# Optimization experiments

Hardware: AMD Instinct MI355X
Metric: run time of the kernel (lower is better)

## Reference

```python
import jax, jax.numpy as jnp
import numpy as np

B, C, H, W = 2048, 512, 4, 4
T, D, NH, HD, FF, NL = 16, 512, 8, 64, 1024, 4
EPS = 1e-5
SCALE = float(1.0 / np.sqrt(HD))


def _make_adj(h, w):
    # torch_geometric.utils.grid(h, w): 3x3 neighborhood incl. self-loop;
    # GCNConv sym-normalizes: A_hat = D^-1/2 A D^-1/2
    n = h * w
    A = np.zeros((n, n), np.float32)
    for r in range(h):
        for c in range(w):
            for dr in (-1, 0, 1):
                for dc in (-1, 0, 1):
                    rr, cc = r + dr, c + dc
                    if 0 <= rr < h and 0 <= cc < w:
                        A[r * w + c, rr * w + cc] = 1.0
    dinv = 1.0 / np.sqrt(A.sum(1))
    return (A * dinv[:, None] * dinv[None, :]).astype(np.float32)


def setup_inputs():
    key = jax.random.key(0)
    ks = iter(jax.random.split(key, 64))
    def w(*s):
        return jax.random.normal(next(ks), s, jnp.float32) * 0.02
    return dict(
        x=jax.random.normal(next(ks), (B, C, H, W), jnp.float32),
        emb_w=w(D, D), emb_b=jnp.zeros((D,), jnp.float32),
        emb_ln_g=jnp.ones((D,), jnp.float32), emb_ln_b=jnp.zeros((D,), jnp.float32),
        pos=w(1, T, D),
        attn_wq=w(NL, D, D), attn_wk=w(NL, D, D), attn_wv=w(NL, D, D),
        attn_bq=jnp.zeros((NL, D), jnp.float32), attn_bk=jnp.zeros((NL, D), jnp.float32),
        attn_bv=jnp.zeros((NL, D), jnp.float32),
        attn_wo=w(NL, D, D), attn_bo=jnp.zeros((NL, D), jnp.float32),
        ln1_g=jnp.ones((NL, D), jnp.float32), ln1_b=jnp.zeros((NL, D), jnp.float32),
        ff_w1=w(NL, D, FF), ff_b1=jnp.zeros((NL, FF), jnp.float32),
        ff_w2=w(NL, FF, D), ff_b2=jnp.zeros((NL, D), jnp.float32),
        ln2_g=jnp.ones((NL, D), jnp.float32), ln2_b=jnp.zeros((NL, D), jnp.float32),
        fc_w=w(D, D), fc_b=jnp.zeros((D,), jnp.float32),
        fc_ln_g=jnp.ones((D,), jnp.float32), fc_ln_b=jnp.zeros((D,), jnp.float32),
        gcn_w1=w(C, 2 * C), gcn_b1=jnp.zeros((2 * C,), jnp.float32),
        gcn_ln1_g=jnp.ones((2 * C,), jnp.float32), gcn_ln1_b=jnp.zeros((2 * C,), jnp.float32),
        gcn_w2=w(2 * C, C), gcn_b2=jnp.zeros((C,), jnp.float32),
        gcn_ln2_g=jnp.ones((C,), jnp.float32), gcn_ln2_b=jnp.zeros((C,), jnp.float32),
        fusion_w=w(C, 2 * C), fusion_b=jnp.zeros((C,), jnp.float32),
        adj=jnp.asarray(_make_adj(H, W)),
    )


def _ln(x, g, b):
    mu = x.mean(-1, keepdims=True)
    var = ((x - mu) ** 2).mean(-1, keepdims=True)
    return (x - mu) * jax.lax.rsqrt(var + EPS) * g + b


def reference(x, emb_w, emb_b, emb_ln_g, emb_ln_b, pos,
              attn_wq, attn_wk, attn_wv, attn_bq, attn_bk, attn_bv, attn_wo, attn_bo,
              ln1_g, ln1_b, ff_w1, ff_b1, ff_w2, ff_b2, ln2_g, ln2_b,
              fc_w, fc_b, fc_ln_g, fc_ln_b,
              gcn_w1, gcn_b1, gcn_ln1_g, gcn_ln1_b, gcn_w2, gcn_b2, gcn_ln2_g, gcn_ln2_b,
              fusion_w, fusion_b, adj):
    Bx = x.shape[0]
    # ---- transformer branch: tokens = 16 spatial positions, dim 512 ----
    h = x.reshape(Bx, C, T).transpose(0, 2, 1)                 # [B,T,D]
    h = _ln(h @ emb_w + emb_b, emb_ln_g, emb_ln_b) + pos
    for i in range(NL):  # post-norm TransformerEncoderLayer, ReLU, eval (no dropout)
        q = (h @ attn_wq[i] + attn_bq[i]).reshape(Bx, T, NH, HD).transpose(0, 2, 1, 3)
        k = (h @ attn_wk[i] + attn_bk[i]).reshape(Bx, T, NH, HD).transpose(0, 2, 1, 3)
        v = (h @ attn_wv[i] + attn_bv[i]).reshape(Bx, T, NH, HD).transpose(0, 2, 1, 3)
        a = jax.nn.softmax(jnp.einsum('bhqd,bhkd->bhqk', q, k) * SCALE, axis=-1)
        o = jnp.einsum('bhqk,bhkd->bhqd', a, v).transpose(0, 2, 1, 3).reshape(Bx, T, D)
        h = _ln(h + o @ attn_wo[i] + attn_bo[i], ln1_g[i], ln1_b[i])
        f = jax.nn.relu(h @ ff_w1[i] + ff_b1[i]) @ ff_w2[i] + ff_b2[i]
        h = _ln(h + f, ln2_g[i], ln2_b[i])
    h = _ln(h @ fc_w + fc_b, fc_ln_g, fc_ln_b)
    x1 = h.transpose(0, 2, 1).reshape(Bx, C, H, W)
    # ---- GCN branch: dense normalized adjacency over the 16-node grid ----
    xn = x.transpose(0, 2, 3, 1).reshape(Bx, T, C)             # [B,16,C]
    g = jnp.einsum('mn,bnd->bmd', adj, xn @ gcn_w1) + gcn_b1   # GCNConv1 (bias after aggr)
    g = jax.nn.elu(_ln(g, gcn_ln1_g, gcn_ln1_b))
    g = jnp.einsum('mn,bnd->bmd', adj, g @ gcn_w2) + gcn_b2    # GCNConv2
    g = jax.nn.elu(_ln(g, gcn_ln2_g, gcn_ln2_b))
    x2 = g.reshape(Bx, H, W, C).transpose(0, 3, 1, 2)
    # ---- fusion: 1x1 conv + InstanceNorm2d (no affine) + ELU ----
    xc = jnp.concatenate([x1, x2], axis=1)                     # [B,2C,H,W]
    y = jnp.einsum('oc,bchw->bohw', fusion_w, xc) + fusion_b[None, :, None, None]
    mu = y.mean((2, 3), keepdims=True)
    var = ((y - mu) ** 2).mean((2, 3), keepdims=True)
    y = (y - mu) * jax.lax.rsqrt(var + EPS)
    return jax.nn.elu(y)
```

## Files before the change

kernel.cpp:

```cpp
#include <hip/hip_runtime.h>


typedef _Float16 f16;
typedef f16 f16x8 __attribute__((ext_vector_type(8)));
typedef f16 f16x4 __attribute__((ext_vector_type(4)));
typedef float f32x4 __attribute__((ext_vector_type(4)));

__device__ inline float wred_sum(float s) {
#pragma unroll
  for (int m = 32; m; m >>= 1) s += __shfl_xor(s, m);
  return s;
}

struct WDesc {
  const float* src;
  f16* dst;
  int K, N, tiles_n, tile_base, mode;
};
struct WTable {
  WDesc d[32];
  int n;
};

__global__ void wconvert_kernel(WTable tab) {
  const int tile = blockIdx.x;
  int di = 0;
  while (di + 1 < tab.n && tab.d[di + 1].tile_base <= tile) ++di;
  const WDesc w = tab.d[di];
  const int t = tile - w.tile_base;
  const int tk = t / w.tiles_n, tn = t % w.tiles_n;
  const int tid = threadIdx.x;
  const int rr = tid >> 5, cc = tid & 31;
  __shared__ float tb[32][33];
  if (w.mode == 0) {
#pragma unroll
    for (int i = 0; i < 4; i++) {
      const int k = tk * 32 + i * 8 + rr, n = tn * 32 + cc;
      tb[i * 8 + rr][cc] = w.src[(size_t)k * w.N + n];
    }
    __syncthreads();
#pragma unroll
    for (int i = 0; i < 4; i++) {
      const int n = tn * 32 + i * 8 + rr, k = tk * 32 + cc;
      w.dst[(size_t)n * w.K + k] = (f16)tb[cc][i * 8 + rr];
    }
  } else {
#pragma unroll
    for (int i = 0; i < 4; i++) {
      const int k = tk * 32 + i * 8 + rr, n = tn * 32 + cc;
      w.dst[(size_t)k * w.N + n] = (f16)w.src[(size_t)k * w.N + n];
    }
  }
}

__global__ void biaspack_kernel(const float* __restrict__ bq,
                                const float* __restrict__ bk,
                                const float* __restrict__ bv,
                                float* __restrict__ bqkv) {
  const int i = blockIdx.x * 256 + threadIdx.x;
  if (i >= 4 * 1536) return;
  const int l = i / 1536, j = i % 1536;
  float v;
  if (j < 512)       v = bq[l * 512 + j];
  else if (j < 1024) v = bk[l * 512 + j - 512];
  else               v = bv[l * 512 + j - 1024];
  bqkv[i] = v;
}

__global__ void prep_kernel(const float* __restrict__ x, f16* __restrict__ X0) {
  const int b = blockIdx.x;
  for (int c = threadIdx.x; c < 512; c += 256) {
    const float* src = x + ((size_t)b * 512 + c) * 16;
    float vals[16];
#pragma unroll
    for (int i = 0; i < 4; i++) {
      const float4 v = ((const float4*)src)[i];
      vals[i * 4 + 0] = v.x; vals[i * 4 + 1] = v.y;
      vals[i * 4 + 2] = v.z; vals[i * 4 + 3] = v.w;
    }
#pragma unroll
    for (int t = 0; t < 16; t++)
      X0[((size_t)b * 16 + t) * 512 + c] = (f16)vals[t];
  }
}

#define STAGE_SLOT(TI, ISB, HALF)                                              \
  {                                                                            \
    f16* dstb_ = smw + ((TI) & 1) * 32768 + ((ISB) ? 16384 : 0) +              \
                 (HALF) * 8192 + ldsw2;                                        \
    const int ld_ = (ISB) ? ldb : lda;                                         \
    const f16* src_ = ((ISB) ? gBs : gAs) + (size_t)((HALF) * 128) * ld_ +     \
                      ((size_t)(TI) << 6);                                     \
    __builtin_amdgcn_global_load_lds(                                          \
        (const __attribute__((address_space(1))) void*)(src_),                 \
        (__attribute__((address_space(3))) void*)(dstb_), 16, 0, 0);           \
    __builtin_amdgcn_global_load_lds(                                          \
        (const __attribute__((address_space(1))) void*)(src_ + (size_t)64 * ld_), \
        (__attribute__((address_space(3))) void*)(dstb_ + 4096), 16, 0, 0);    \
  }

#define VM4 asm volatile("s_waitcnt vmcnt(4)" ::: "memory");
#define VM0 asm volatile("s_waitcnt vmcnt(0)" ::: "memory");
#define VMN

#define PHASE(TI, P, FIRST, DOSTG, STI, SISB, SHALF, VM)                       \
  {                                                                            \
    const f16* Ab_ = smw + ((TI) & 1) * 32768;                                 \
    const f16* Bb_ = Ab_ + 16384;                                              \
    if (FIRST) {                                                               \
      _Pragma("unroll") for (int n = 0; n < 4; ++n) {                          \
        const int r = wn + n * 16 + rm;                                        \
        bf[n][0] = *(const f16x8*)(Bb_ + r * 64 + koff0);                      \
        bf[n][1] = *(const f16x8*)(Bb_ + r * 64 + koff1);                      \
      }                                                                        \
    }                                                                          \
    const int r0_ = wm + (2 * (P)) * 16 + rm;                                  \
    const f16x8 a0k0 = *(const f16x8*)(Ab_ + r0_ * 64 + koff0);                \
    const f16x8 a0k1 = *(const f16x8*)(Ab_ + r0_ * 64 + koff1);                \
    const f16x8 a1k0 = *(const f16x8*)(Ab_ + (r0_ + 16) * 64 + koff0);         \
    const f16x8 a1k1 = *(const f16x8*)(Ab_ + (r0_ + 16) * 64 + koff1);         \
    if (DOSTG) STAGE_SLOT(STI, SISB, SHALF)                                    \
    VM                                                                         \
    __builtin_amdgcn_s_barrier();                                              \
    asm volatile("s_waitcnt lgkmcnt(0)" ::: "memory");                         \
    __builtin_amdgcn_sched_barrier(0);                                         \
    __builtin_amdgcn_s_setprio(1);                                             \
    _Pragma("unroll") for (int n = 0; n < 4; ++n) {                            \
      acc[2 * (P)][n] = __builtin_amdgcn_mfma_f32_16x16x32_f16(                \
          a0k0, bf[n][0], acc[2 * (P)][n], 0, 0, 0);                           \
      acc[2 * (P)][n] = __builtin_amdgcn_mfma_f32_16x16x32_f16(                \
          a0k1, bf[n][1], acc[2 * (P)][n], 0, 0, 0);                           \
      acc[2 * (P) + 1][n] = __builtin_amdgcn_mfma_f32_16x16x32_f16(            \
          a1k0, bf[n][0], acc[2 * (P) + 1][n], 0, 0, 0);                       \
      acc[2 * (P) + 1][n] = __builtin_amdgcn_mfma_f32_16x16x32_f16(            \
          a1k1, bf[n][1], acc[2 * (P) + 1][n], 0, 0, 0);                       \
    }                                                                          \
    __builtin_amdgcn_s_setprio(0);                                             \
    __builtin_amdgcn_s_barrier();                                              \
    __builtin_amdgcn_sched_barrier(0);                                         \
  }

template <int OUT, bool RELU, bool HASB, int NT>
__global__ __launch_bounds__(512) void gemm256_kernel(
    const f16* __restrict__ A, const f16* __restrict__ Bt, void* __restrict__ C,
    const float* __restrict__ bias, const f16* __restrict__ resp,
    int N, int lda, int ldb) {
  __shared__ alignas(16) f16 smem[65536];
  f16* smw = smem;
  const int tid = threadIdx.x;
  const int nb = N >> 8;
  const int cpx = gridDim.x >> 3;
  const int wg = (blockIdx.x & 7) * cpx + (blockIdx.x >> 3);
  const int bx = wg % nb, by = wg / nb;
  const int row0 = by << 8, col0 = bx << 8;
  const int lane = tid & 63;
  const int wid = tid >> 6;
  const int wm = (wid >> 2) << 7;
  const int wn = (wid & 3) << 6;
  const int rm = lane & 15;
  const int kg = lane >> 4;
  const int key = rm & 7;
  const int koff0 = ((kg ^ key)) << 3;
  const int koff1 = (((4 + kg) ^ key)) << 3;
  const int schunk = (tid & 7) ^ ((tid >> 3) & 7);
  const f16* gAs = A + (size_t)(row0 + (tid >> 3)) * lda + (schunk << 3);
  const f16* gBs = Bt + (size_t)(col0 + (tid >> 3)) * ldb + (schunk << 3);
  const int ldsw2 = (tid & 0x1C0) << 3;
  f32x4 acc[8][4] = {};
  f16x8 bf[4][2];

  STAGE_SLOT(0, 0, 0)
  STAGE_SLOT(0, 0, 1)
  STAGE_SLOT(0, 1, 0)
  STAGE_SLOT(0, 1, 1)
  STAGE_SLOT(1, 1, 0)
  STAGE_SLOT(1, 1, 1)
  VM4
  __builtin_amdgcn_s_barrier();
  __builtin_amdgcn_sched_barrier(0);

#pragma unroll 1
  for (int j = 0; j < NT / 2 - 1; ++j) {
    const int u = 2 * j, v = u + 1, t2 = u + 2, t3 = u + 3;
    PHASE(u, 0, true,  true, v,  0, 0, VMN)
    PHASE(u, 1, false, true, v,  0, 1, VMN)
    PHASE(u, 2, false, true, t2, 1, 0, VMN)
    PHASE(u, 3, false, true, t2, 1, 1, VM4)
    PHASE(v, 0, true,  true, t2, 0, 0, VMN)
    PHASE(v, 1, false, true, t2, 0, 1, VMN)
    PHASE(v, 2, false, true, t3, 1, 0, VMN)
    PHASE(v, 3, false, true, t3, 1, 1, VM4)
  }
  {
    const int u = NT - 2, v = NT - 1;
    PHASE(u, 0, true,  true,  v, 0, 0, VMN)
    PHASE(u, 1, false, true,  v, 0, 1, VMN)
    PHASE(u, 2, false, false, 0, 0, 0, VMN)
    PHASE(u, 3, false, false, 0, 0, 0, VM0)
    PHASE(v, 0, true,  false, 0, 0, 0, VMN)
    PHASE(v, 1, false, false, 0, 0, 0, VMN)
    PHASE(v, 2, false, false, 0, 0, 0, VMN)
    PHASE(v, 3, false, false, 0, 0, 0, VMN)
  }

  const int cn = lane & 15;
  const int rg = (lane >> 4) << 2;
  if (OUT == 3) {
    float* out = (float*)C;
#pragma unroll
    for (int m = 0; m < 8; ++m) {
      const int bidx = (row0 >> 4) + (wm >> 4) + m;
#pragma unroll
      for (int n = 0; n < 4; ++n) {
        const int col = col0 + wn + n * 16 + cn;
        const float v0 = acc[m][n][0], v1 = acc[m][n][1];
        const float v2 = acc[m][n][2], v3 = acc[m][n][3];
        float s = v0 + v1 + v2 + v3;
        s += __shfl_xor(s, 16);
        s += __shfl_xor(s, 32);
        const float mu = s * (1.f / 16.f);
        float q = (v0 - mu) * (v0 - mu) + (v1 - mu) * (v1 - mu) +
                  (v2 - mu) * (v2 - mu) + (v3 - mu) * (v3 - mu);
        q += __shfl_xor(q, 16);
        q += __shfl_xor(q, 32);
        const float rstd = rsqrtf(q * (1.f / 16.f) + 1e-5f);
        float4 z;
        z.x = (v0 - mu) * rstd; z.x = z.x > 0.f ? z.x : expm1f(z.x);
        z.y = (v1 - mu) * rstd; z.y = z.y > 0.f ? z.y : expm1f(z.y);
        z.z = (v2 - mu) * rstd; z.z = z.z > 0.f ? z.z : expm1f(z.z);
        z.w = (v3 - mu) * rstd; z.w = z.w > 0.f ? z.w : expm1f(z.w);
        *(float4*)(out + ((size_t)bidx * 512 + col) * 16 + rg) = z;
      }
    }
  } else {
#pragma unroll
    for (int m = 0; m < 8; ++m) {
#pragma unroll
      for (int n = 0; n < 4; ++n) {
        const int col = col0 + wn + n * 16 + cn;
        const float bv = HASB ? bias[col] : 0.0f;
#pragma unroll
        for (int r = 0; r < 4; ++r) {
          const int row = row0 + wm + m * 16 + rg + r;
          float v = acc[m][n][r] + bv;
          if (OUT == 4) v += (float)resp[(size_t)row * N + col];
          if (RELU) v = v > 0.f ? v : 0.f;
          ((f16*)C)[(size_t)row * N + col] = (f16)v;
        }
      }
    }
  }
}

template <bool RES, bool POS>
__global__ void ln_kernel(const f16* in, const f16* res, const float* g,
                          const float* b, const float* pos, f16* out) {
  const int row = (blockIdx.x << 2) + (threadIdx.x >> 6);
  const int lane = threadIdx.x & 63;
  const int c0 = lane << 3;
  float v[8];
  const f16x8 xi = *(const f16x8*)(in + (size_t)row * 512 + c0);
  if (RES) {
    const f16x8 ri = *(const f16x8*)(res + (size_t)row * 512 + c0);
#pragma unroll
    for (int j = 0; j < 8; j++) v[j] = (float)xi[j] + (float)ri[j];
  } else {
#pragma unroll
    for (int j = 0; j < 8; j++) v[j] = (float)xi[j];
  }
  float s = 0;
#pragma unroll
  for (int j = 0; j < 8; j++) s += v[j];
  s = wred_sum(s);
  const float mu = s * (1.f / 512.f);
  float q = 0;
#pragma unroll
  for (int j = 0; j < 8; j++) {
    const float d = v[j] - mu;
    q += d * d;
  }
  q = wred_sum(q);
  const float rstd = rsqrtf(q * (1.f / 512.f) + 1e-5f);
  const int t = row & 15;
  f16x8 o8;
#pragma unroll
  for (int j = 0; j < 8; j++) {
    float o = (v[j] - mu) * rstd * g[c0 + j] + b[c0 + j];
    if (POS) o += pos[t * 512 + c0 + j];
    o8[j] = (f16)o;
  }
  *(f16x8*)(out + (size_t)row * 512 + c0) = o8;
}

__global__ void lnpack_kernel(const f16* __restrict__ in, const f16* __restrict__ x2,
                              const float* __restrict__ g, const float* __restrict__ b,
                              f16* __restrict__ F) {
  const int row = (blockIdx.x << 2) + (threadIdx.x >> 6);
  const int lane = threadIdx.x & 63;
  const int c0 = lane << 3;
  const f16x8 xi = *(const f16x8*)(in + (size_t)row * 512 + c0);
  float v[8];
#pragma unroll
  for (int j = 0; j < 8; j++) v[j] = (float)xi[j];
  float s = 0;
#pragma unroll
  for (int j = 0; j < 8; j++) s += v[j];
  s = wred_sum(s);
  const float mu = s * (1.f / 512.f);
  float q = 0;
#pragma unroll
  for (int j = 0; j < 8; j++) {
    const float d = v[j] - mu;
    q += d * d;
  }
  q = wred_sum(q);
  const float rstd = rsqrtf(q * (1.f / 512.f) + 1e-5f);
  f16x8 o8;
#pragma unroll
  for (int j = 0; j < 8; j++)
    o8[j] = (f16)((v[j] - mu) * rstd * g[c0 + j] + b[c0 + j]);
  *(f16x8*)(F + (size_t)row * 1024 + c0) = o8;
  const f16x8 x2v = *(const f16x8*)(x2 + (size_t)row * 512 + c0);
  *(f16x8*)(F + (size_t)row * 1024 + 512 + c0) = x2v;
}

__global__ __launch_bounds__(256) void attn_kernel(const f16* __restrict__ qkv,
                                                   f16* __restrict__ o) {
  __shared__ f16 smem[4][3776];
  const int wid = threadIdx.x >> 6;
  const int lane = threadIdx.x & 63;
  const int bh = (blockIdx.x << 2) + wid;
  const int b = bh >> 3, h = bh & 7;
  f16* W = smem[wid];
  f16* Qw = W;
  f16* Kw = W + 1152;
  f16* Vw = W + 2304;
  f16* Pw = W + 3456;
  const size_t base = (size_t)b * 24576 + (size_t)h * 64;
#pragma unroll
  for (int i = 0; i < 6; i++) {
    const int c = i * 64 + lane;
    const int t = c / 24;
    const int rem = c - t * 24;
    const int mat = rem >> 3, ch = rem & 7;
    const f16x8 v = *(const f16x8*)(qkv + base + (size_t)t * 1536 + mat * 512 + ch * 8);
    *(f16x8*)(W + mat * 1152 + t * 72 + ch * 8) = v;
  }
  __syncthreads();
  const int rm = lane & 15, kg = lane >> 4;
  f32x4 s4 = {};
  {
    const f16x8 q0 = *(const f16x8*)(Qw + rm * 72 + kg * 8);
    const f16x8 q1 = *(const f16x8*)(Qw + rm * 72 + 32 + kg * 8);
    const f16x8 k0 = *(const f16x8*)(Kw + rm * 72 + kg * 8);
    const f16x8 k1 = *(const f16x8*)(Kw + rm * 72 + 32 + kg * 8);
    s4 = __builtin_amdgcn_mfma_f32_16x16x32_f16(q0, k0, s4, 0, 0, 0);
    s4 = __builtin_amdgcn_mfma_f32_16x16x32_f16(q1, k1, s4, 0, 0, 0);
  }
  float p[4];
#pragma unroll
  for (int r = 0; r < 4; r++) {
    const float sv = s4[r] * 0.125f;
    float m = sv;
    m = fmaxf(m, __shfl_xor(m, 1));
    m = fmaxf(m, __shfl_xor(m, 2));
    m = fmaxf(m, __shfl_xor(m, 4));
    m = fmaxf(m, __shfl_xor(m, 8));
    const float e = expf(sv - m);
    float s = e;
    s += __shfl_xor(s, 1);
    s += __shfl_xor(s, 2);
    s += __shfl_xor(s, 4);
    s += __shfl_xor(s, 8);
    p[r] = e / s;
  }
#pragma unroll
  for (int r = 0; r < 4; r++) Pw[(kg * 4 + r) * 20 + rm] = (f16)p[r];
  __syncthreads();
  const f16x4 pa = *(const f16x4*)(Pw + rm * 20 + kg * 4);
  f32x4 o4[4] = {};
#pragma unroll
  for (int dt = 0; dt < 4; dt++) {
    f16x4 vb;
#pragma unroll
    for (int kk = 0; kk < 4; kk++) vb[kk] = Vw[(kg * 4 + kk) * 72 + dt * 16 + rm];
    o4[dt] = __builtin_amdgcn_mfma_f32_16x16x16f16(pa, vb, o4[dt], 0, 0, 0);
  }
  f16* op = o + (size_t)b * 16 * 512 + (size_t)h * 64;
#pragma unroll
  for (int dt = 0; dt < 4; dt++)
#pragma unroll
    for (int r = 0; r < 4; r++)
      op[(size_t)(kg * 4 + r) * 512 + dt * 16 + rm] = (f16)o4[dt][r];
}

template <int DG>
__global__ __launch_bounds__(256) void adjmix_kernel(
    const f16* __restrict__ r, const float* __restrict__ adj,
    const float* __restrict__ bias, const float* __restrict__ g,
    const float* __restrict__ bet, f16* __restrict__ out, int ldo) {
  const int b = blockIdx.x;
  const int tid = threadIdx.x;
  __shared__ float agg[16][DG];
  __shared__ float adjs[256];
  if (tid < 256) adjs[tid] = adj[tid];
  __syncthreads();
  const int d0 = tid * 4;
  if (d0 < DG) {
    float acc[16][4];
#pragma unroll
    for (int m = 0; m < 16; m++)
#pragma unroll
      for (int j = 0; j < 4; j++) acc[m][j] = 0.f;
#pragma unroll
    for (int n = 0; n < 16; n++) {
      const f16x4 v = *(const f16x4*)(r + ((size_t)b * 16 + n) * DG + d0);
      const float v0 = (float)v[0], v1 = (float)v[1], v2 = (float)v[2], v3 = (float)v[3];
#pragma unroll
      for (int m = 0; m < 16; m++) {
        const float a = adjs[m * 16 + n];
        acc[m][0] += a * v0;
        acc[m][1] += a * v1;
        acc[m][2] += a * v2;
        acc[m][3] += a * v3;
      }
    }
    const float4 bv = *(const float4*)(bias + d0);
#pragma unroll
    for (int m = 0; m < 16; m++) {
      agg[m][d0 + 0] = acc[m][0] + bv.x;
      agg[m][d0 + 1] = acc[m][1] + bv.y;
      agg[m][d0 + 2] = acc[m][2] + bv.z;
      agg[m][d0 + 3] = acc[m][3] + bv.w;
    }
  }
  __syncthreads();
  const int wave = tid >> 6, lane = tid & 63;
  for (int m = wave; m < 16; m += 4) {
    float s = 0;
#pragma unroll
    for (int j = 0; j < DG / 64; j++) s += agg[m][j * 64 + lane];
    s = wred_sum(s);
    const float mu = s / DG;
    float q = 0;
#pragma unroll
    for (int j = 0; j < DG / 64; j++) {
      const float t = agg[m][j * 64 + lane] - mu;
      q += t * t;
    }
    q = wred_sum(q);
    const float rstd = rsqrtf(q / DG + 1e-5f);
    const size_t grow = (size_t)b * 16 + m;
#pragma unroll
    for (int j = 0; j < DG / 64; j++) {
      const int d = j * 64 + lane;
      float v = (agg[m][d] - mu) * rstd * g[d] + bet[d];
      v = v > 0.f ? v : expm1f(v);
      out[grow * ldo + d] = (f16)v;
    }
  }
}

extern "C" void kernel_launch(void* const* d_in, const int* in_sizes, int n_in,
                              void* d_out, int out_size, void* d_ws, size_t ws_size,
                              hipStream_t stream) {
  (void)in_sizes; (void)n_in; (void)out_size; (void)ws_size;
  const float* x         = (const float*)d_in[0];
  const float* emb_w     = (const float*)d_in[1];
  const float* emb_b     = (const float*)d_in[2];
  const float* emb_ln_g  = (const float*)d_in[3];
  const float* emb_ln_b  = (const float*)d_in[4];
  const float* pos       = (const float*)d_in[5];
  const float* attn_wq   = (const float*)d_in[6];
  const float* attn_wk   = (const float*)d_in[7];
  const float* attn_wv   = (const float*)d_in[8];
  const float* attn_bq   = (const float*)d_in[9];
  const float* attn_bk   = (const float*)d_in[10];
  const float* attn_bv   = (const float*)d_in[11];
  const float* attn_wo   = (const float*)d_in[12];
  const float* attn_bo   = (const float*)d_in[13];
  const float* ln1_g     = (const float*)d_in[14];
  const float* ln1_b     = (const float*)d_in[15];
  const float* ff_w1     = (const float*)d_in[16];
  const float* ff_b1     = (const float*)d_in[17];
  const float* ff_w2     = (const float*)d_in[18];
  const float* ff_b2     = (const float*)d_in[19];
  const float* ln2_g     = (const float*)d_in[20];
  const float* ln2_b     = (const float*)d_in[21];
  const float* fc_w      = (const float*)d_in[22];
  const float* fc_b      = (const float*)d_in[23];
  const float* fc_ln_g   = (const float*)d_in[24];
  const float* fc_ln_b   = (const float*)d_in[25];
  const float* gcn_w1    = (const float*)d_in[26];
  const float* gcn_b1    = (const float*)d_in[27];
  const float* gcn_ln1_g = (const float*)d_in[28];
  const float* gcn_ln1_b = (const float*)d_in[29];
  const float* gcn_w2    = (const float*)d_in[30];
  const float* gcn_b2    = (const float*)d_in[31];
  const float* gcn_ln2_g = (const float*)d_in[32];
  const float* gcn_ln2_b = (const float*)d_in[33];
  const float* fusion_w  = (const float*)d_in[34];
  const float* fusion_b  = (const float*)d_in[35];
  const float* adj       = (const float*)d_in[36];
  (void)fusion_b;

  char* ws = (char*)d_ws;
  f16*   WF   = (f16*)(ws);
  float* BQKV = (float*)(ws + 20971520ull);
  f16*   Ap   = (f16*)(ws + 20996096ull);
  f16*   Bp   = (f16*)(ws + 54550528ull);
  f16*   Cp   = (f16*)(ws + 88104960ull);
  f16*   Qp   = (f16*)(ws + 121659392ull);

  const size_t o_emb = 0, o_qkv = 262144, o_wo = 3407872, o_ff1 = 4456448,
               o_ff2 = 6553600, o_fc = 8650752, o_g1 = 8912896, o_g2 = 9437184,
               o_fus = 9961472;

  WTable tab{};
  int ntab = 0, tbase = 0;
  auto add = [&](const float* s, f16* dst, int K, int N, int mode) {
    WDesc& w = tab.d[ntab++];
    w.src = s; w.dst = dst; w.K = K; w.N = N;
    w.tiles_n = N / 32; w.tile_base = tbase; w.mode = mode;
    tbase += (K / 32) * (N / 32);
  };
  add(emb_w, WF + o_emb, 512, 512, 0);
  for (int l = 0; l < 4; l++) {
    add(attn_wq + l * 262144, WF + o_qkv + (size_t)l * 786432, 512, 512, 0);
    add(attn_wk + l * 262144, WF + o_qkv + (size_t)l * 786432 + 262144, 512, 512, 0);
    add(attn_wv + l * 262144, WF + o_qkv + (size_t)l * 786432 + 524288, 512, 512, 0);
  }
  for (int l = 0; l < 4; l++)
    add(attn_wo + l * 262144, WF + o_wo + (size_t)l * 262144, 512, 512, 0);
  for (int l = 0; l < 4; l++)
    add(ff_w1 + l * 524288, WF + o_ff1 + (size_t)l * 524288, 512, 1024, 0);
  for (int l = 0; l < 4; l++)
    add(ff_w2 + l * 524288, WF + o_ff2 + (size_t)l * 524288, 1024, 512, 0);
  add(fc_w, WF + o_fc, 512, 512, 0);
  add(gcn_w1, WF + o_g1, 512, 1024, 0);
  add(gcn_w2, WF + o_g2, 1024, 512, 0);
  add(fusion_w, WF + o_fus, 512, 1024, 1);
  tab.n = ntab;

  wconvert_kernel<<<tbase, 256, 0, stream>>>(tab);
  biaspack_kernel<<<24, 256, 0, stream>>>(attn_bq, attn_bk, attn_bv, BQKV);
  prep_kernel<<<2048, 256, 0, stream>>>(x, Ap);

  gemm256_kernel<0, false, false, 8><<<512, 512, 0, stream>>>(
      Ap, WF + o_g1, Qp, nullptr, nullptr, 1024, 512, 512);
  adjmix_kernel<1024><<<2048, 256, 0, stream>>>(
      Qp, adj, gcn_b1, gcn_ln1_g, gcn_ln1_b, Bp, 1024);
  gemm256_kernel<0, false, false, 16><<<256, 512, 0, stream>>>(
      Bp, WF + o_g2, Qp, nullptr, nullptr, 512, 1024, 1024);

  gemm256_kernel<0, false, true, 8><<<256, 512, 0, stream>>>(
      Ap, WF + o_emb, Cp, emb_b, nullptr, 512, 512, 512);
  ln_kernel<false, true><<<8192, 256, 0, stream>>>(
      Cp, nullptr, emb_ln_g, emb_ln_b, pos, Bp);

  adjmix_kernel<512><<<2048, 256, 0, stream>>>(
      Qp, adj, gcn_b2, gcn_ln2_g, gcn_ln2_b, Ap, 512);

  for (int i = 0; i < 4; i++) {
    gemm256_kernel<0, false, true, 8><<<768, 512, 0, stream>>>(
        Bp, WF + o_qkv + (size_t)i * 786432, Qp, BQKV + i * 1536, nullptr,
        1536, 512, 512);
    attn_kernel<<<4096, 256, 0, stream>>>(Qp, Cp);
    gemm256_kernel<4, false, true, 8><<<256, 512, 0, stream>>>(
        Cp, WF + o_wo + (size_t)i * 262144, Qp, attn_bo + i * 512, Bp,
        512, 512, 512);
    ln_kernel<false, false><<<8192, 256, 0, stream>>>(
        Qp, nullptr, ln1_g + i * 512, ln1_b + i * 512, nullptr, Bp);
    gemm256_kernel<0, true, true, 8><<<512, 512, 0, stream>>>(
        Bp, WF + o_ff1 + (size_t)i * 524288, Qp, ff_b1 + i * 1024, nullptr,
        1024, 512, 512);
    gemm256_kernel<4, false, true, 16><<<256, 512, 0, stream>>>(
        Qp, WF + o_ff2 + (size_t)i * 524288, Qp + 33554432ull, ff_b2 + i * 512,
        Bp, 512, 1024, 1024);
    ln_kernel<false, false><<<8192, 256, 0, stream>>>(
        Qp + 33554432ull, nullptr, ln2_g + i * 512, ln2_b + i * 512, nullptr, Bp);
  }

  gemm256_kernel<0, false, true, 8><<<256, 512, 0, stream>>>(
      Bp, WF + o_fc, Qp, fc_b, nullptr, 512, 512, 512);
  lnpack_kernel<<<8192, 256, 0, stream>>>(Qp, Ap, fc_ln_g, fc_ln_b, Bp);

  gemm256_kernel<3, false, false, 16><<<256, 512, 0, stream>>>(
      Bp, WF + o_fus, d_out, nullptr, nullptr, 512, 1024, 1024);
}
```

Before: 1.291 ms.

## Fuse LayerNorm into full-row 64x512 GEMM epilogue for emb, Wo and FF2

Adds a GEMM kernel whose tiles cover 64 rows by the full 512-column width, so the epilogue can compute row mean and variance with shuffles and a small shared-memory reduction. It then applies the LayerNorm, plus the residual or positional add, before writing. This replaces the 256-tile GEMM followed by a separate LN kernel for the embedding, attention output and FF2 projections. The aim is to remove the intermediate fp16 write and re-read and the extra launches. In exchange, each block re-streams the whole weight matrix, data reuse of B is lower, variance uses E[x^2]-mu^2 in fp32, and the output is written in place over the residual buffer.

```diff
diff --git a/kernel.cpp b/kernel.cpp
--- a/kernel.cpp
+++ b/kernel.cpp
@@ -252,44 +252,152 @@
   }
 }
 
-template <bool RES, bool POS>
-__global__ void ln_kernel(const f16* in, const f16* res, const float* g,
-                          const float* b, const float* pos, f16* out) {
-  const int row = (blockIdx.x << 2) + (threadIdx.x >> 6);
-  const int lane = threadIdx.x & 63;
-  const int c0 = lane << 3;
-  float v[8];
-  const f16x8 xi = *(const f16x8*)(in + (size_t)row * 512 + c0);
-  if (RES) {
-    const f16x8 ri = *(const f16x8*)(res + (size_t)row * 512 + c0);
-#pragma unroll
-    for (int j = 0; j < 8; j++) v[j] = (float)xi[j] + (float)ri[j];
-  } else {
-#pragma unroll
-    for (int j = 0; j < 8; j++) v[j] = (float)xi[j];
-  }
-  float s = 0;
-#pragma unroll
-  for (int j = 0; j < 8; j++) s += v[j];
-  s = wred_sum(s);
-  const float mu = s * (1.f / 512.f);
-  float q = 0;
-#pragma unroll
-  for (int j = 0; j < 8; j++) {
-    const float d = v[j] - mu;
-    q += d * d;
-  }
-  q = wred_sum(q);
-  const float rstd = rsqrtf(q * (1.f / 512.f) + 1e-5f);
-  const int t = row & 15;
-  f16x8 o8;
-#pragma unroll
-  for (int j = 0; j < 8; j++) {
-    float o = (v[j] - mu) * rstd * g[c0 + j] + b[c0 + j];
-    if (POS) o += pos[t * 512 + c0 + j];
-    o8[j] = (f16)o;
-  }
-  *(f16x8*)(out + (size_t)row * 512 + c0) = o8;
+template <int LNMODE, int NT>
+__global__ __launch_bounds__(512) void gemm64ln_kernel(
+    const f16* __restrict__ A, const f16* __restrict__ Bt, f16* __restrict__ outp,
+    const float* __restrict__ bias, const f16* resp,
+    const float* __restrict__ g, const float* __restrict__ bvec,
+    const float* __restrict__ pos, int lda) {
+  constexpr int K = NT * 32;
+  __shared__ alignas(16) f16 smem[2][18432];
+  const int tid = threadIdx.x;
+  const int cpx = gridDim.x >> 3;
+  const int wg = (blockIdx.x & 7) * cpx + (blockIdx.x >> 3);
+  const int row0 = wg << 6;
+  const int lane = tid & 63;
+  const int wid = tid >> 6;
+  const int wn = wid << 6;
+  const int rm = lane & 15;
+  const int kg = lane >> 4;
+  const int koff = (kg ^ ((rm >> 1) & 3)) << 3;
+  const int srow = tid >> 2;
+  const int schunk = (tid & 3) ^ ((tid >> 3) & 3);
+  const f16* gAs = A + (size_t)(row0 + srow) * lda + (schunk << 3);
+  const f16* gBs = Bt + (size_t)srow * K + (schunk << 3);
+  const int ldsw = (tid & 0x1C0) << 3;
+  f32x4 acc[4][4] = {};
+
+  auto STAGE = [&](int t) {
+    f16* buf = smem[t & 1];
+    const int kt = t << 5;
+    if (tid < 256)
+      __builtin_amdgcn_global_load_lds(
+          (const __attribute__((address_space(1))) void*)(gAs + kt),
+          (__attribute__((address_space(3))) void*)(buf + ldsw), 16, 0, 0);
+#pragma unroll
+    for (int i = 0; i < 4; ++i)
+      __builtin_amdgcn_global_load_lds(
+          (const __attribute__((address_space(1))) void*)(gBs + (size_t)(i * 128) * K + kt),
+          (__attribute__((address_space(3))) void*)(buf + 2048 + i * 4096 + ldsw),
+          16, 0, 0);
+  };
+
+  STAGE(0);
+  asm volatile("s_waitcnt vmcnt(0)" ::: "memory");
+  __builtin_amdgcn_s_barrier();
+  __builtin_amdgcn_sched_barrier(0);
+
+#pragma unroll 1
+  for (int t = 0; t < NT; ++t) {
+    if (t + 1 < NT) STAGE(t + 1);
+    const f16* buf = smem[t & 1];
+    f16x8 af[4], bf[4];
+#pragma unroll
+    for (int n = 0; n < 4; ++n)
+      bf[n] = *(const f16x8*)(buf + 2048 + ((wn + n * 16 + rm) << 5) + koff);
+#pragma unroll
+    for (int m = 0; m < 4; ++m)
+      af[m] = *(const f16x8*)(buf + ((m * 16 + rm) << 5) + koff);
+    __builtin_amdgcn_s_setprio(1);
+#pragma unroll
+    for (int m = 0; m < 4; ++m)
+#pragma unroll
+      for (int n = 0; n < 4; ++n)
+        acc[m][n] =
+            __builtin_amdgcn_mfma_f32_16x16x32_f16(af[m], bf[n], acc[m][n], 0, 0, 0);
+    __builtin_amdgcn_s_setprio(0);
+    if (t + 1 < NT) {
+      asm volatile("s_waitcnt vmcnt(0)" ::: "memory");
+      __builtin_amdgcn_s_barrier();
+      __builtin_amdgcn_sched_barrier(0);
+    }
+  }
+
+  const int cn = lane & 15;
+  const int rg = (lane >> 4) << 2;
+  float biasn[4];
+#pragma unroll
+  for (int n = 0; n < 4; ++n) biasn[n] = bias[wn + n * 16 + cn];
+#pragma unroll
+  for (int m = 0; m < 4; ++m)
+#pragma unroll
+    for (int n = 0; n < 4; ++n) {
+      const int col = wn + n * 16 + cn;
+#pragma unroll
+      for (int r = 0; r < 4; ++r) {
+        float val = acc[m][n][r] + biasn[n];
+        if (LNMODE == 1)
+          val += (float)resp[(size_t)(row0 + m * 16 + rg + r) * 512 + col];
+        acc[m][n][r] = val;
+      }
+    }
+  float* part = (float*)smem;
+  __syncthreads();
+#pragma unroll
+  for (int m = 0; m < 4; ++m)
+#pragma unroll
+    for (int r = 0; r < 4; ++r) {
+      float s = 0, q = 0;
+#pragma unroll
+      for (int n = 0; n < 4; ++n) {
+        const float val = acc[m][n][r];
+        s += val;
+        q += val * val;
+      }
+      s += __shfl_xor(s, 1); s += __shfl_xor(s, 2);
+      s += __shfl_xor(s, 4); s += __shfl_xor(s, 8);
+      q += __shfl_xor(q, 1); q += __shfl_xor(q, 2);
+      q += __shfl_xor(q, 4); q += __shfl_xor(q, 8);
+      if (cn == 0) {
+        part[(m * 16 + rg + r) * 16 + wid * 2] = s;
+        part[(m * 16 + rg + r) * 16 + wid * 2 + 1] = q;
+      }
+    }
+  __syncthreads();
+  float mu_[4][4], rs_[4][4];
+#pragma unroll
+  for (int m = 0; m < 4; ++m)
+#pragma unroll
+    for (int r = 0; r < 4; ++r) {
+      const int row = m * 16 + rg + r;
+      float S = 0, Q = 0;
+#pragma unroll
+      for (int w = 0; w < 8; ++w) {
+        S += part[row * 16 + w * 2];
+        Q += part[row * 16 + w * 2 + 1];
+      }
+      const float mu = S * (1.f / 512.f);
+      mu_[m][r] = mu;
+      rs_[m][r] = rsqrtf(Q * (1.f / 512.f) - mu * mu + 1e-5f);
+    }
+  float gv[4], bv2[4];
+#pragma unroll
+  for (int n = 0; n < 4; ++n) {
+    gv[n] = g[wn + n * 16 + cn];
+    bv2[n] = bvec[wn + n * 16 + cn];
+  }
+#pragma unroll
+  for (int m = 0; m < 4; ++m)
+#pragma unroll
+    for (int n = 0; n < 4; ++n) {
+      const int col = wn + n * 16 + cn;
+#pragma unroll
+      for (int r = 0; r < 4; ++r) {
+        float o = (acc[m][n][r] - mu_[m][r]) * rs_[m][r] * gv[n] + bv2[n];
+        if (LNMODE == 2) o += pos[(rg + r) * 512 + col];
+        outp[(size_t)(row0 + m * 16 + rg + r) * 512 + col] = (f16)o;
+      }
+    }
 }
 
 __global__ void lnpack_kernel(const f16* __restrict__ in, const f16* __restrict__ x2,
@@ -553,10 +661,8 @@
   gemm256_kernel<0, false, false, 16><<<256, 512, 0, stream>>>(
       Bp, WF + o_g2, Qp, nullptr, nullptr, 512, 1024, 1024);
 
-  gemm256_kernel<0, false, true, 8><<<256, 512, 0, stream>>>(
-      Ap, WF + o_emb, Cp, emb_b, nullptr, 512, 512, 512);
-  ln_kernel<false, true><<<8192, 256, 0, stream>>>(
-      Cp, nullptr, emb_ln_g, emb_ln_b, pos, Bp);
+  gemm64ln_kernel<2, 16><<<512, 512, 0, stream>>>(
+      Ap, WF + o_emb, Bp, emb_b, nullptr, emb_ln_g, emb_ln_b, pos, 512);
 
   adjmix_kernel<512><<<2048, 256, 0, stream>>>(
       Qp, adj, gcn_b2, gcn_ln2_g, gcn_ln2_b, Ap, 512);
@@ -566,19 +672,15 @@
         Bp, WF + o_qkv + (size_t)i * 786432, Qp, BQKV + i * 1536, nullptr,
         1536, 512, 512);
     attn_kernel<<<4096, 256, 0, stream>>>(Qp, Cp);
-    gemm256_kernel<4, false, true, 8><<<256, 512, 0, stream>>>(
-        Cp, WF + o_wo + (size_t)i * 262144, Qp, attn_bo + i * 512, Bp,
-        512, 512, 512);
-    ln_kernel<false, false><<<8192, 256, 0, stream>>>(
-        Qp, nullptr, ln1_g + i * 512, ln1_b + i * 512, nullptr, Bp);
+    gemm64ln_kernel<1, 16><<<512, 512, 0, stream>>>(
+        Cp, WF + o_wo + (size_t)i * 262144, Bp, attn_bo + i * 512, Bp,
+        ln1_g + i * 512, ln1_b + i * 512, nullptr, 512);
     gemm256_kernel<0, true, true, 8><<<512, 512, 0, stream>>>(
         Bp, WF + o_ff1 + (size_t)i * 524288, Qp, ff_b1 + i * 1024, nullptr,
         1024, 512, 512);
-    gemm256_kernel<4, false, true, 16><<<256, 512, 0, stream>>>(
-        Qp, WF + o_ff2 + (size_t)i * 524288, Qp + 33554432ull, ff_b2 + i * 512,
-        Bp, 512, 1024, 1024);
-    ln_kernel<false, false><<<8192, 256, 0, stream>>>(
-        Qp + 33554432ull, nullptr, ln2_g + i * 512, ln2_b + i * 512, nullptr, Bp);
+    gemm64ln_kernel<1, 32><<<512, 512, 0, stream>>>(
+        Qp, WF + o_ff2 + (size_t)i * 524288, Bp, ff_b2 + i * 512, Bp,
+        ln2_g + i * 512, ln2_b + i * 512, nullptr, 1024);
   }
 
   gemm256_kernel<0, false, true, 8><<<256, 512, 0, stream>>>(
```

Result: slower. 1.445 ms (+11.9%).

## Fold LayerNorms into following GEMMs using row stats computed in-kernel

Applied to the files above, without the earlier changes.

Removes the standalone LayerNorm kernels after attention-out and FFN-out. The LN gamma is folded into the next weight matrix during conversion, and the beta/bias terms go into precomputed column vectors. The consuming GEMM accumulates per-row sum and sum-of-squares of its f16 A input during the main loop and applies the normalization in its epilogue. The residual GEMMs then rebuild the normalized residual from stored stats. This cuts several full activation read/write passes per layer, but adds VALU work in the MFMA loop and uses the less stable E[x^2]-mu^2 variance form.

```diff
diff --git a/kernel.cpp b/kernel.cpp
--- a/kernel.cpp
+++ b/kernel.cpp
@@ -14,6 +14,7 @@
 
 struct WDesc {
   const float* src;
+  const float* gs;
   f16* dst;
   int K, N, tiles_n, tile_base, mode;
 };
@@ -42,7 +43,8 @@
 #pragma unroll
     for (int i = 0; i < 4; i++) {
       const int n = tn * 32 + i * 8 + rr, k = tk * 32 + cc;
-      w.dst[(size_t)n * w.K + k] = (f16)tb[cc][i * 8 + rr];
+      const float gv = w.gs ? w.gs[k] : 1.0f;
+      w.dst[(size_t)n * w.K + k] = (f16)(tb[cc][i * 8 + rr] * gv);
     }
   } else {
 #pragma unroll
@@ -51,6 +53,35 @@
       w.dst[(size_t)k * w.N + n] = (f16)w.src[(size_t)k * w.N + n];
     }
   }
+}
+
+struct FDesc {
+  const float* W;
+  const float* g;
+  const float* be;
+  const float* bias;
+  int N, ld, coff, doff, obase;
+};
+struct FTable {
+  FDesc d[16];
+  int n;
+};
+
+__global__ void foldvec_kernel(FTable tab, float* __restrict__ CD) {
+  const int gid = blockIdx.x * 256 + threadIdx.x;
+  int di = 0;
+  while (di + 1 < tab.n && tab.d[di + 1].obase <= gid) ++di;
+  const FDesc f = tab.d[di];
+  const int n = gid - f.obase;
+  if (n >= f.N) return;
+  float c = 0.f, d = 0.f;
+  for (int k = 0; k < 512; ++k) {
+    const float w = f.W[(size_t)k * f.ld + n];
+    c += f.be[k] * w;
+    d += f.g[k] * w;
+  }
+  CD[f.coff + n] = c + f.bias[n];
+  CD[f.doff + n] = d;
 }
 
 __global__ void biaspack_kernel(const float* __restrict__ bq,
@@ -136,14 +167,26 @@
           a1k1, bf[n][1], acc[2 * (P) + 1][n], 0, 0, 0);                       \
     }                                                                          \
     __builtin_amdgcn_s_setprio(0);                                             \
+    if (STATS && (wid & 3) == 0) {                                             \
+      _Pragma("unroll") for (int e = 0; e < 8; ++e) {                          \
+        const float v0_ = (float)a0k0[e], v1_ = (float)a0k1[e];                \
+        const float v2_ = (float)a1k0[e], v3_ = (float)a1k1[e];                \
+        rs[2 * (P)] += v0_ + v1_;                                              \
+        rq[2 * (P)] += v0_ * v0_ + v1_ * v1_;                                  \
+        rs[2 * (P) + 1] += v2_ + v3_;                                          \
+        rq[2 * (P) + 1] += v2_ * v2_ + v3_ * v3_;                              \
+      }                                                                        \
+    }                                                                          \
     __builtin_amdgcn_s_barrier();                                              \
     __builtin_amdgcn_sched_barrier(0);                                         \
   }
 
-template <int OUT, bool RELU, bool HASB, int NT>
+template <int OUT, bool RELU, bool HASB, int NT, bool STATS>
 __global__ __launch_bounds__(512) void gemm256_kernel(
     const f16* __restrict__ A, const f16* __restrict__ Bt, void* __restrict__ C,
     const float* __restrict__ bias, const f16* __restrict__ resp,
+    const float* __restrict__ aux1, const float* __restrict__ aux2,
+    const float* __restrict__ statsIn, float* __restrict__ statsOut,
     int N, int lda, int ldb) {
   __shared__ alignas(16) f16 smem[65536];
   f16* smw = smem;
@@ -168,6 +211,7 @@
   const int ldsw2 = (tid & 0x1C0) << 3;
   f32x4 acc[8][4] = {};
   f16x8 bf[4][2];
+  float rs[8] = {}, rq[8] = {};
 
   STAGE_SLOT(0, 0, 0)
   STAGE_SLOT(0, 0, 1)
@@ -205,6 +249,25 @@
 
   const int cn = lane & 15;
   const int rg = (lane >> 4) << 2;
+  float* ldsStats = (float*)smw;
+  if (STATS) {
+    if ((wid & 3) == 0) {
+#pragma unroll
+      for (int p2 = 0; p2 < 8; ++p2) {
+        float s = rs[p2], q = rq[p2];
+        s += __shfl_xor(s, 16); s += __shfl_xor(s, 32);
+        q += __shfl_xor(q, 16); q += __shfl_xor(q, 32);
+        if (lane < 16) {
+          const int lr = wm + p2 * 16 + lane;
+          ldsStats[lr * 2] = s;
+          ldsStats[lr * 2 + 1] = q;
+          *(float2*)(statsOut + (size_t)(row0 + lr) * 2) = make_float2(s, q);
+        }
+      }
+    }
+    __syncthreads();
+  }
+
   if (OUT == 3) {
     float* out = (float*)C;
 #pragma unroll
@@ -230,6 +293,44 @@
         z.z = (v2 - mu) * rstd; z.z = z.z > 0.f ? z.z : expm1f(z.z);
         z.w = (v3 - mu) * rstd; z.w = z.w > 0.f ? z.w : expm1f(z.w);
         *(float4*)(out + ((size_t)bidx * 512 + col) * 16 + rg) = z;
+      }
+    }
+  } else if (OUT == 5) {
+#pragma unroll
+    for (int m = 0; m < 8; ++m) {
+#pragma unroll
+      for (int r = 0; r < 4; ++r) {
+        const int lr = wm + m * 16 + rg + r;
+        const float mu = ldsStats[lr * 2] * (1.f / 512.f);
+        const float rr2 =
+            rsqrtf(ldsStats[lr * 2 + 1] * (1.f / 512.f) - mu * mu + 1e-5f);
+        const size_t row = (size_t)row0 + lr;
+#pragma unroll
+        for (int n = 0; n < 4; ++n) {
+          const int col = col0 + wn + n * 16 + cn;
+          float v = rr2 * (acc[m][n][r] - mu * aux2[col]) + aux1[col];
+          if (RELU) v = v > 0.f ? v : 0.f;
+          ((f16*)C)[row * N + col] = (f16)v;
+        }
+      }
+    }
+  } else if (OUT == 6) {
+#pragma unroll
+    for (int m = 0; m < 8; ++m) {
+#pragma unroll
+      for (int r = 0; r < 4; ++r) {
+        const size_t row = (size_t)row0 + wm + m * 16 + rg + r;
+        const float s_ = statsIn[row * 2], q_ = statsIn[row * 2 + 1];
+        const float mu = s_ * (1.f / 512.f);
+        const float rr2 = rsqrtf(q_ * (1.f / 512.f) - mu * mu + 1e-5f);
+#pragma unroll
+        for (int n = 0; n < 4; ++n) {
+          const int col = col0 + wn + n * 16 + cn;
+          const float yv = (float)resp[row * N + col];
+          const float v =
+              acc[m][n][r] + bias[col] + (yv - mu) * rr2 * aux1[col] + aux2[col];
+          ((f16*)C)[row * N + col] = (f16)v;
+        }
       }
     }
   } else {
@@ -511,6 +612,9 @@
   f16*   Bp   = (f16*)(ws + 54550528ull);
   f16*   Cp   = (f16*)(ws + 88104960ull);
   f16*   Qp   = (f16*)(ws + 121659392ull);
+  float* S1   = (float*)(ws + 222322688ull);
+  float* S2   = (float*)(ws + 222584832ull);
+  float* CD   = (float*)(ws + 222846976ull);
 
   const size_t o_emb = 0, o_qkv = 262144, o_wo = 3407872, o_ff1 = 4456448,
                o_ff2 = 6553600, o_fc = 8650752, o_g1 = 8912896, o_g2 = 9437184,
@@ -518,43 +622,72 @@
 
   WTable tab{};
   int ntab = 0, tbase = 0;
-  auto add = [&](const float* s, f16* dst, int K, int N, int mode) {
+  auto add = [&](const float* s, const float* gs, f16* dst, int K, int N, int mode) {
     WDesc& w = tab.d[ntab++];
-    w.src = s; w.dst = dst; w.K = K; w.N = N;
+    w.src = s; w.gs = gs; w.dst = dst; w.K = K; w.N = N;
     w.tiles_n = N / 32; w.tile_base = tbase; w.mode = mode;
     tbase += (K / 32) * (N / 32);
   };
-  add(emb_w, WF + o_emb, 512, 512, 0);
+  add(emb_w, nullptr, WF + o_emb, 512, 512, 0);
   for (int l = 0; l < 4; l++) {
-    add(attn_wq + l * 262144, WF + o_qkv + (size_t)l * 786432, 512, 512, 0);
-    add(attn_wk + l * 262144, WF + o_qkv + (size_t)l * 786432 + 262144, 512, 512, 0);
-    add(attn_wv + l * 262144, WF + o_qkv + (size_t)l * 786432 + 524288, 512, 512, 0);
+    const float* gs = (l >= 1) ? (ln2_g + (l - 1) * 512) : nullptr;
+    add(attn_wq + l * 262144, gs, WF + o_qkv + (size_t)l * 786432, 512, 512, 0);
+    add(attn_wk + l * 262144, gs, WF + o_qkv + (size_t)l * 786432 + 262144, 512, 512, 0);
+    add(attn_wv + l * 262144, gs, WF + o_qkv + (size_t)l * 786432 + 524288, 512, 512, 0);
   }
   for (int l = 0; l < 4; l++)
-    add(attn_wo + l * 262144, WF + o_wo + (size_t)l * 262144, 512, 512, 0);
+    add(attn_wo + l * 262144, nullptr, WF + o_wo + (size_t)l * 262144, 512, 512, 0);
   for (int l = 0; l < 4; l++)
-    add(ff_w1 + l * 524288, WF + o_ff1 + (size_t)l * 524288, 512, 1024, 0);
+    add(ff_w1 + l * 524288, ln1_g + l * 512, WF + o_ff1 + (size_t)l * 524288, 512, 1024, 0);
   for (int l = 0; l < 4; l++)
-    add(ff_w2 + l * 524288, WF + o_ff2 + (size_t)l * 524288, 1024, 512, 0);
-  add(fc_w, WF + o_fc, 512, 512, 0);
-  add(gcn_w1, WF + o_g1, 512, 1024, 0);
-  add(gcn_w2, WF + o_g2, 1024, 512, 0);
-  add(fusion_w, WF + o_fus, 512, 1024, 1);
+    add(ff_w2 + l * 524288, nullptr, WF + o_ff2 + (size_t)l * 524288, 1024, 512, 0);
+  add(fc_w, ln2_g + 3 * 512, WF + o_fc, 512, 512, 0);
+  add(gcn_w1, nullptr, WF + o_g1, 512, 1024, 0);
+  add(gcn_w2, nullptr, WF + o_g2, 1024, 512, 0);
+  add(fusion_w, nullptr, WF + o_fus, 512, 1024, 1);
   tab.n = ntab;
+
+  FTable ft{};
+  int nf = 0, ob = 0;
+  auto fadd = [&](const float* W, const float* g, const float* be,
+                  const float* bias, int N, int ld, int coff, int doff) {
+    FDesc& f = ft.d[nf++];
+    f.W = W; f.g = g; f.be = be; f.bias = bias;
+    f.N = N; f.ld = ld; f.coff = coff; f.doff = doff; f.obase = ob;
+    ob += N;
+  };
+  for (int l = 0; l < 4; l++)
+    fadd(ff_w1 + l * 524288, ln1_g + l * 512, ln1_b + l * 512,
+         ff_b1 + l * 1024, 1024, 1024, l * 2048, l * 2048 + 1024);
+  for (int l = 1; l < 4; l++) {
+    const int c0 = 8192 + (l - 1) * 3072, d0 = c0 + 1536;
+    fadd(attn_wq + l * 262144, ln2_g + (l - 1) * 512, ln2_b + (l - 1) * 512,
+         attn_bq + l * 512, 512, 512, c0 + 0, d0 + 0);
+    fadd(attn_wk + l * 262144, ln2_g + (l - 1) * 512, ln2_b + (l - 1) * 512,
+         attn_bk + l * 512, 512, 512, c0 + 512, d0 + 512);
+    fadd(attn_wv + l * 262144, ln2_g + (l - 1) * 512, ln2_b + (l - 1) * 512,
+         attn_bv + l * 512, 512, 512, c0 + 1024, d0 + 1024);
+  }
+  fadd(fc_w, ln2_g + 3 * 512, ln2_b + 3 * 512, fc_b, 512, 512, 17408, 17920);
+  ft.n = nf;
 
   wconvert_kernel<<<tbase, 256, 0, stream>>>(tab);
   biaspack_kernel<<<24, 256, 0, stream>>>(attn_bq, attn_bk, attn_bv, BQKV);
+  foldvec_kernel<<<36, 256, 0, stream>>>(ft, CD);
   prep_kernel<<<2048, 256, 0, stream>>>(x, Ap);
 
-  gemm256_kernel<0, false, false, 8><<<512, 512, 0, stream>>>(
-      Ap, WF + o_g1, Qp, nullptr, nullptr, 1024, 512, 512);
+  gemm256_kernel<0, false, false, 8, false><<<512, 512, 0, stream>>>(
+      Ap, WF + o_g1, Qp, nullptr, nullptr, nullptr, nullptr, nullptr, nullptr,
+      1024, 512, 512);
   adjmix_kernel<1024><<<2048, 256, 0, stream>>>(
       Qp, adj, gcn_b1, gcn_ln1_g, gcn_ln1_b, Bp, 1024);
-  gemm256_kernel<0, false, false, 16><<<256, 512, 0, stream>>>(
-      Bp, WF + o_g2, Qp, nullptr, nullptr, 512, 1024, 1024);
-
-  gemm256_kernel<0, false, true, 8><<<256, 512, 0, stream>>>(
-      Ap, WF + o_emb, Cp, emb_b, nullptr, 512, 512, 512);
+  gemm256_kernel<0, false, false, 16, false><<<256, 512, 0, stream>>>(
+      Bp, WF + o_g2, Qp, nullptr, nullptr, nullptr, nullptr, nullptr, nullptr,
+      512, 1024, 1024);
+
+  gemm256_kernel<0, false, true, 8, false><<<256, 512, 0, stream>>>(
+      Ap, WF + o_emb, Cp, emb_b, nullptr, nullptr, nullptr, nullptr, nullptr,
+      512, 512, 512);
   ln_kernel<false, true><<<8192, 256, 0, stream>>>(
       Cp, nullptr, emb_ln_g, emb_ln_b, pos, Bp);
 
@@ -562,29 +695,41 @@
       Qp, adj, gcn_b2, gcn_ln2_g, gcn_ln2_b, Ap, 512);
 
   for (int i = 0; i < 4; i++) {
-    gemm256_kernel<0, false, true, 8><<<768, 512, 0, stream>>>(
-        Bp, WF + o_qkv + (size_t)i * 786432, Qp, BQKV + i * 1536, nullptr,
-        1536, 512, 512);
+    if (i == 0) {
+      gemm256_kernel<0, false, true, 8, false><<<768, 512, 0, stream>>>(
+          Bp, WF + o_qkv, Qp, BQKV, nullptr, nullptr, nullptr, nullptr, nullptr,
+          1536, 512, 512);
+    } else {
+      const int c0 = 8192 + (i - 1) * 3072;
+      gemm256_kernel<5, false, false, 8, true><<<768, 512, 0, stream>>>(
+          Bp, WF + o_qkv + (size_t)i * 786432, Qp, nullptr, nullptr,
+          CD + c0, CD + c0 + 1536, nullptr, S1, 1536, 512, 512);
+    }
     attn_kernel<<<4096, 256, 0, stream>>>(Qp, Cp);
-    gemm256_kernel<4, false, true, 8><<<256, 512, 0, stream>>>(
-        Cp, WF + o_wo + (size_t)i * 262144, Qp, attn_bo + i * 512, Bp,
-        512, 512, 512);
-    ln_kernel<false, false><<<8192, 256, 0, stream>>>(
-        Qp, nullptr, ln1_g + i * 512, ln1_b + i * 512, nullptr, Bp);
-    gemm256_kernel<0, true, true, 8><<<512, 512, 0, stream>>>(
-        Bp, WF + o_ff1 + (size_t)i * 524288, Qp, ff_b1 + i * 1024, nullptr,
-        1024, 512, 512);
-    gemm256_kernel<4, false, true, 16><<<256, 512, 0, stream>>>(
-        Qp, WF + o_ff2 + (size_t)i * 524288, Qp + 33554432ull, ff_b2 + i * 512,
-        Bp, 512, 1024, 1024);
-    ln_kernel<false, false><<<8192, 256, 0, stream>>>(
-        Qp + 33554432ull, nullptr, ln2_g + i * 512, ln2_b + i * 512, nullptr, Bp);
-  }
-
-  gemm256_kernel<0, false, true, 8><<<256, 512, 0, stream>>>(
-      Bp, WF + o_fc, Qp, fc_b, nullptr, 512, 512, 512);
+    if (i == 0) {
+      gemm256_kernel<4, false, true, 8, false><<<256, 512, 0, stream>>>(
+          Cp, WF + o_wo, Bp, attn_bo, Bp, nullptr, nullptr, nullptr, nullptr,
+          512, 512, 512);
+    } else {
+      gemm256_kernel<6, false, true, 8, false><<<256, 512, 0, stream>>>(
+          Cp, WF + o_wo + (size_t)i * 262144, Bp, attn_bo + i * 512, Bp,
+          ln2_g + (i - 1) * 512, ln2_b + (i - 1) * 512, S1, nullptr,
+          512, 512, 512);
+    }
+    gemm256_kernel<5, true, false, 8, true><<<512, 512, 0, stream>>>(
+        Bp, WF + o_ff1 + (size_t)i * 524288, Qp, nullptr, nullptr,
+        CD + i * 2048, CD + i * 2048 + 1024, nullptr, S2, 1024, 512, 512);
+    gemm256_kernel<6, false, true, 16, false><<<256, 512, 0, stream>>>(
+        Qp, WF + o_ff2 + (size_t)i * 524288, Bp, ff_b2 + i * 512, Bp,
+        ln1_g + i * 512, ln1_b + i * 512, S2, nullptr, 512, 1024, 1024);
+  }
+
+  gemm256_kernel<5, false, false, 8, true><<<256, 512, 0, stream>>>(
+      Bp, WF + o_fc, Qp, nullptr, nullptr, CD + 17408, CD + 17920, nullptr, S1,
+      512, 512, 512);
   lnpack_kernel<<<8192, 256, 0, stream>>>(Qp, Ap, fc_ln_g, fc_ln_b, Bp);
 
-  gemm256_kernel<3, false, false, 16><<<256, 512, 0, stream>>>(
-      Bp, WF + o_fus, d_out, nullptr, nullptr, 512, 1024, 1024);
-}
+  gemm256_kernel<3, false, false, 16, false><<<256, 512, 0, stream>>>(
+      Bp, WF + o_fus, d_out, nullptr, nullptr, nullptr, nullptr, nullptr,
+      nullptr, 512, 1024, 1024);
+}
```

New measurement: 1.573 ms. +21.9%, slower.
